# Kernel tuning notes

Hardware: AMD Instinct MI355X
Metric: run time of the kernel (lower is better)

## Reference

```python
import jax, jax.numpy as jnp
import numpy as np

B, S, BERT_H = 8, 512, 432
NL, HD = 12, 64
H = NL * HD  # 768
NEG = -1e12

def _lin(k, i, o):
    return jax.random.normal(k, (i, o), jnp.float32) * 0.02

def setup_inputs():
    key = jax.random.key(0)
    ks = jax.random.split(key, 12)
    return {
        "bert_hidden": jax.random.normal(ks[0], (B, S, BERT_H), jnp.float32),
        "attention_mask": jnp.ones((B, S), jnp.float32),
        "dense_w": _lin(ks[1], BERT_H, H), "dense_b": jnp.zeros((H,)),
        "sat_qw": _lin(ks[2], H, H), "sat_qb": jnp.zeros((H,)),
        "sat_kw": _lin(ks[3], H, H), "sat_kb": jnp.zeros((H,)),
        "sat_vw": _lin(ks[4], H, H), "sat_vb": jnp.zeros((H,)),
        "sat_ow": _lin(ks[5], H, H), "sat_ob": jnp.zeros((H,)),
        "rel_qw": _lin(ks[6], H, H), "rel_qb": jnp.zeros((H,)),
        "rel_kw": _lin(ks[7], H, H), "rel_kb": jnp.zeros((H,)),
        "rel_vw": _lin(ks[8], H, H), "rel_vb": jnp.zeros((H,)),
        "rel_ow": _lin(ks[9], H, H), "rel_ob": jnp.zeros((H,)),
        "lns_w": jnp.ones((H,)), "lns_b": jnp.zeros((H,)),
        "lnr_w": jnp.ones((H,)), "lnr_b": jnp.zeros((H,)),
        "head_w": _lin(ks[10], H, 2 * HD), "head_b": jnp.zeros((2 * HD,)),
        "tail_w": _lin(ks[11], 2 * HD, 2 * NL), "tail_b": jnp.zeros((2 * NL,)),
    }

def _layernorm(x, w, b, eps=1e-12):
    u = x.mean(-1, keepdims=True)
    s = ((x - u) ** 2).mean(-1, keepdims=True)
    return w * (x - u) / jnp.sqrt(s + eps) + b

def _mha(q_in, k_in, v_in, wq, bq, wk, bk, wv, bv, wo, bo):
    # q_in: [N, Lq, H]; k_in/v_in: [N, Lk, H]; dropout is identity (eval)
    N, Lq, _ = q_in.shape
    Lk = k_in.shape[1]
    qh = (q_in @ wq + bq).reshape(N, Lq, NL, HD)
    kh = (k_in @ wk + bk).reshape(N, Lk, NL, HD)
    vh = (v_in @ wv + bv).reshape(N, Lk, NL, HD)
    scores = jnp.einsum('nqhd,nkhd->nhqk', qh, kh) / np.float32(np.sqrt(HD))
    probs = jax.nn.softmax(scores, axis=-1)
    ctx = jnp.einsum('nhqk,nkhd->nqhd', probs, vh).reshape(N, Lq, NL * HD)
    return ctx @ wo + bo + q_in

def _shift_back(x):
    # faithful torch cycle_shift(forward=False): circular roll left by 1
    return jnp.roll(x, -1, axis=1)

def _shift_fwd(x):
    # faithful to the torch sequential in-place loop in cycle_shift(forward=True):
    # out[0] = x[-1]; out[1:] = x[0] (each copy reads the already-overwritten slot)
    b, s, h = x.shape
    return jnp.concatenate([x[:, -1:, :], jnp.broadcast_to(x[:, :1, :], (b, s - 1, h))], axis=1)

def reference(bert_hidden, attention_mask, dense_w, dense_b,
              sat_qw, sat_qb, sat_kw, sat_kb, sat_vw, sat_vb, sat_ow, sat_ob,
              rel_qw, rel_qb, rel_kw, rel_kb, rel_vw, rel_vb, rel_ow, rel_ob,
              lns_w, lns_b, lnr_w, lnr_b, head_w, head_b, tail_w, tail_b):
    hidden0 = bert_hidden @ dense_w + dense_b  # [B,S,H]
    cs = hidden0
    center = cs.mean(axis=1)  # [B,H], avg_pool2d over seq dim
    for _ in range(2):
        before = _shift_back(cs)
        after = _shift_fwd(cs)
        center_exp = jnp.broadcast_to(center[:, None, :], cs.shape)
        concats = jnp.stack([before, cs, after, hidden0, center_exp], axis=2)  # [B,S,5,H]
        concats = concats.reshape(B * S, 5, H)
        q = cs.reshape(B * S, 1, H)
        sat = _mha(q, concats, concats, sat_qw, sat_qb, sat_kw, sat_kb, sat_vw, sat_vb, sat_ow, sat_ob)
        cs = _layernorm(jax.nn.relu(sat), lns_w, lns_b).reshape(B, S, H)
        cc = jnp.concatenate([center[:, None, :], cs], axis=1)  # [B,S+1,H]
        rel = _mha(center[:, None, :], cc, cc, rel_qw, rel_qb, rel_kw, rel_kb, rel_vw, rel_vb, rel_ow, rel_ob)
        center = _layernorm(jax.nn.relu(rel), lnr_w, lnr_b)[:, 0, :]
    outputs = cs @ head_w + head_b  # [B,S,2*HD]
    qw, kw = outputs[..., ::2], outputs[..., 1::2]  # [B,S,HD]
    pos = jnp.arange(S, dtype=jnp.float32)
    inv = jnp.power(10000.0, -2.0 * jnp.arange(HD // 2, dtype=jnp.float32) / HD)
    ang = pos[:, None] * inv[None, :]  # [S,HD//2]
    pe = jnp.stack([jnp.sin(ang), jnp.cos(ang)], axis=-1).reshape(S, HD)
    cos_pos = jnp.repeat(pe[:, 1::2], 2, axis=-1)  # [S,HD]
    sin_pos = jnp.repeat(pe[:, ::2], 2, axis=-1)
    def rot(x):
        x2 = jnp.stack([-x[..., 1::2], x[..., ::2]], axis=-1).reshape(x.shape)
        return x * cos_pos + x2 * sin_pos
    qw, kw = rot(qw), rot(kw)
    logits = jnp.einsum('bmd,bnd->bmn', qw, kw) / np.float32(np.sqrt(HD))  # [B,S,S]
    bias = jnp.einsum('bnh->bhn', outputs @ tail_w + tail_b) / 2.0  # [B,2*NL,S]
    logits = logits[:, None, :, :] + bias[:, ::2, None, :] + bias[:, 1::2, :, None]  # [B,NL,S,S]
    m1 = attention_mask[:, None, :, None]
    logits = logits * m1 + NEG * (1.0 - m1)
    m2 = attention_mask[:, None, None, :]
    logits = logits * m2 + NEG * (1.0 - m2)
    tril = jnp.tril(jnp.ones((S, S), logits.dtype), k=-1)
    return logits - tril * 1e12
```

## Files before the change

kernel.cpp:

```cpp
#include <hip/hip_runtime.h>
#include <cstdint>
#include <cstddef>

#define HH 768
#define SS 512
#define NBATCH 8
#define NLH 12
#define HDIM 64
#define BSROWS 4096
static constexpr float NEGV = -1000000000000.0f;

typedef unsigned short ushort_t;
typedef __attribute__((ext_vector_type(4))) float fx4;
typedef __attribute__((ext_vector_type(8))) short sx8;

__device__ __forceinline__ ushort_t f2bf(float f) {
  uint32_t u = __float_as_uint(f);
  uint32_t r = (u + 0x7FFFu + ((u >> 16) & 1u)) >> 16;
  return (ushort_t)r;
}
__device__ __forceinline__ float bf2f(ushort_t h) {
  return __uint_as_float(((uint32_t)h) << 16);
}
__device__ __forceinline__ float2 ldbf2(const ushort_t* p) {
  uint32_t u = *(const uint32_t*)p;
  return make_float2(__uint_as_float(u << 16), __uint_as_float(u & 0xffff0000u));
}

__device__ __forceinline__ void async_copy16(void* lds, const void* g) {
  __builtin_amdgcn_global_load_lds(
      (const __attribute__((address_space(1))) void*)g,
      (__attribute__((address_space(3))) void*)lds, 16, 0, 0);
}

__device__ __forceinline__ void gemm_core(
    char* arena, int bid, int nwg, int nx,
    const ushort_t* __restrict__ A, int lda,
    const ushort_t* __restrict__ B, int ldb,
    const float* __restrict__ bias,
    const ushort_t* __restrict__ resb,
    ushort_t* __restrict__ Cb, int ldo,
    ushort_t* __restrict__ Cb2, int ldo2, int nsplit, int K,
    float* __restrict__ colmean)
{
  ushort_t* As = (ushort_t*)arena;
  ushort_t* Bs = (ushort_t*)(arena + 16384);
  const int tid = threadIdx.x;
  const int q = nwg >> 3;
  const int xcd = bid & 7, sidx = bid >> 3;
  const int swz = xcd * q + sidx;
  const int bm = (swz / nx) * 128;
  const int bn = (swz % nx) * 128;
  const int l = tid & 63;
  const int w = tid >> 6;
  const int wr = w >> 1, wc = w & 1;
  const int r8 = tid >> 3;
  const int sl = tid & 7;

  fx4 acc[4][4];
#pragma unroll
  for (int m = 0; m < 4; ++m)
#pragma unroll
    for (int n = 0; n < 4; ++n) acc[m][n] = (fx4)0.f;

  for (int k0 = 0; k0 < K; k0 += 64) {
#pragma unroll
    for (int i = 0; i < 4; ++i) {
      int row = i * 32 + r8;
      int srcs = sl ^ (row & 7);
      async_copy16((char*)As + i * 4096 + tid * 16,
                   A + (size_t)(bm + row) * lda + k0 + srcs * 8);
    }
#pragma unroll
    for (int i = 0; i < 4; ++i) {
      int row = i * 32 + r8;
      int srcs = sl ^ (row & 7);
      async_copy16((char*)Bs + i * 4096 + tid * 16,
                   B + (size_t)(bn + row) * ldb + k0 + srcs * 8);
    }
    __syncthreads();
#pragma unroll
    for (int kk = 0; kk < 2; ++kk) {
      sx8 av[4], bv[4];
      const int so = (l >> 4) + kk * 4;
#pragma unroll
      for (int m = 0; m < 4; ++m) {
        int r = wr * 64 + m * 16 + (l & 15);
        av[m] = *(const sx8*)((const char*)As + r * 128 + ((so ^ (r & 7)) * 16));
      }
#pragma unroll
      for (int n = 0; n < 4; ++n) {
        int r = wc * 64 + n * 16 + (l & 15);
        bv[n] = *(const sx8*)((const char*)Bs + r * 128 + ((so ^ (r & 7)) * 16));
      }
#pragma unroll
      for (int m = 0; m < 4; ++m)
#pragma unroll
        for (int n = 0; n < 4; ++n)
          acc[m][n] = __builtin_amdgcn_mfma_f32_16x16x32_bf16(av[m], bv[n], acc[m][n], 0, 0, 0);
    }
    __syncthreads();
  }

  const bool second = (bn >= nsplit);
  ushort_t* dst = second ? Cb2 : Cb;
  const int ld = second ? ldo2 : ldo;
  const int csub = second ? nsplit : 0;
  const int cr0 = bm + wr * 64 + (l >> 4) * 4;
  const int cc0 = bn + wc * 64 + (l & 15);
#pragma unroll
  for (int m = 0; m < 4; ++m) {
#pragma unroll
    for (int n = 0; n < 4; ++n) {
      int col = cc0 + n * 16;
      float bcol = bias[col];
#pragma unroll
      for (int j = 0; j < 4; ++j) {
        int row = cr0 + m * 16 + j;
        size_t off = (size_t)row * ld + (col - csub);
        float v = acc[m][n][j] + bcol;
        if (resb) v += bf2f(resb[off]);
        dst[off] = f2bf(v);
      }
    }
  }

  if (colmean) {
    float* scr = (float*)arena;
    const int cid = wr * 4 + (l >> 4);
#pragma unroll
    for (int n = 0; n < 4; ++n) {
      int colL = wc * 64 + n * 16 + (l & 15);
      float t = 16.0f * bias[bn + colL];
#pragma unroll
      for (int m = 0; m < 4; ++m)
#pragma unroll
        for (int j = 0; j < 4; ++j) t += acc[m][n][j];
      scr[cid * 128 + colL] = t;
    }
    __syncthreads();
    if (tid < 128) {
      float scol = 0.f;
#pragma unroll
      for (int c = 0; c < 8; ++c) scol += scr[c * 128 + tid];
      atomicAdd(&colmean[(bm >> 9) * HH + bn + tid], scol * (1.0f / 512.0f));
    }
  }
}

struct SmallJob { const float* W; const float* bias; const float* res; float* C; };
struct SmallJobs { SmallJob j[5]; };

__device__ __forceinline__ void skinny_core(
    char* arena, int colblk,
    const float* __restrict__ A, const float* __restrict__ W,
    const float* __restrict__ bias, const float* __restrict__ res, float* __restrict__ C)
{
  float* As = (float*)arena;
  float* part = (float*)(arena + 24576);
  const int tid = threadIdx.x;
#pragma unroll
  for (int i = 0; i < 6; ++i) {
    int idx = tid * 4 + i * 1024;
    *(float4*)&As[idx] = *(const float4*)(A + idx);
  }
  __syncthreads();
  const int c = tid & 31;
  const int col = (colblk << 5) + c;
  const int ks = tid >> 5;
  const float* Wp = W + (size_t)(ks * 96) * HH + col;
  float acc[8] = {};
#pragma unroll 8
  for (int k = 0; k < 96; ++k) {
    float wv = Wp[(size_t)k * HH];
    const float* ap = &As[ks * 96 + k];
#pragma unroll
    for (int m = 0; m < 8; ++m)
      acc[m] = fmaf(ap[m * HH], wv, acc[m]);
  }
#pragma unroll
  for (int m = 0; m < 8; ++m)
    part[ks * 256 + m * 32 + c] = acc[m];
  __syncthreads();
  const int m = tid >> 5;
  const int c2 = tid & 31;
  float s = 0.f;
#pragma unroll
  for (int k = 0; k < 8; ++k) s += part[k * 256 + m * 32 + c2];
  const int outcol = (colblk << 5) + c2;
  float v = s + bias[outcol];
  if (res) v += res[(size_t)m * HH + outcol];
  C[(size_t)m * HH + outcol] = v;
}

__global__ __launch_bounds__(256) void gemm_bf16(
    const ushort_t* __restrict__ A, int lda,
    const ushort_t* __restrict__ B, int ldb,
    const float* __restrict__ bias,
    const ushort_t* __restrict__ resb,
    ushort_t* __restrict__ Cb, int ldo,
    ushort_t* __restrict__ Cb2, int ldo2, int nsplit, int K, int nx,
    float* __restrict__ colmean)
{
  __shared__ char arena[32768];
  gemm_core(arena, blockIdx.x, gridDim.x, nx, A, lda, B, ldb, bias, resb,
            Cb, ldo, Cb2, ldo2, nsplit, K, colmean);
}

__global__ __launch_bounds__(256) void qkv_center(
    const ushort_t* __restrict__ A, const ushort_t* __restrict__ B,
    const float* __restrict__ bias, ushort_t* __restrict__ Cb,
    SmallJobs jobs, const float* __restrict__ center)
{
  __shared__ char arena[32768];
  if (blockIdx.x < 576) {
    gemm_core(arena, blockIdx.x, 576, 18, A, HH, B, HH, bias, nullptr,
              Cb, 2304, nullptr, 0, 1 << 30, HH, nullptr);
  } else {
    int vb = blockIdx.x - 576;
    SmallJob jb = jobs.j[vb / 24];
    skinny_core(arena, vb % 24, center, jb.W, jb.bias, jb.res, jb.C);
  }
}

__global__ __launch_bounds__(256) void gemm_skinny(
    const float* __restrict__ A, SmallJobs jobs)
{
  __shared__ char arena[32768];
  SmallJob jb = jobs.j[blockIdx.y];
  skinny_core(arena, blockIdx.x, A, jb.W, jb.bias, jb.res, jb.C);
}

struct SmallJobs2 { SmallJob j[2]; };
__global__ __launch_bounds__(256) void skinny_ln(
    const float* __restrict__ relo, const float* __restrict__ lw, const float* __restrict__ lb,
    SmallJobs2 jobs)
{
  __shared__ float As[8 * HH];
  __shared__ float part[8 * 8 * 32];
  const int tid = threadIdx.x;
  const SmallJob job = jobs.j[blockIdx.y];
#pragma unroll
  for (int i = 0; i < 6; ++i) {
    int idx = tid * 4 + i * 1024;
    *(float4*)&As[idx] = *(const float4*)(relo + idx);
  }
  __syncthreads();
  {
    const int row = tid >> 5, lc = tid & 31;
    float s = 0.f, sq = 0.f;
#pragma unroll
    for (int e = 0; e < 24; ++e) {
      float x = fmaxf(As[row * HH + lc * 24 + e], 0.f);
      s += x; sq += x * x;
    }
#pragma unroll
    for (int d = 1; d < 32; d <<= 1) { s += __shfl_xor(s, d); sq += __shfl_xor(sq, d); }
    float mean = s * (1.0f / HH);
    float var = sq * (1.0f / HH) - mean * mean;
    float rstd = rsqrtf(var + 1e-12f);
#pragma unroll
    for (int e = 0; e < 24; ++e) {
      int cc = lc * 24 + e;
      float x = fmaxf(As[row * HH + cc], 0.f);
      As[row * HH + cc] = lw[cc] * (x - mean) * rstd + lb[cc];
    }
  }
  __syncthreads();
  const int c = tid & 31;
  const int col = (blockIdx.x << 5) + c;
  const int ks = tid >> 5;
  const float* Wp = job.W + (size_t)(ks * 96) * HH + col;
  float acc[8] = {};
#pragma unroll 8
  for (int k = 0; k < 96; ++k) {
    float wv = Wp[(size_t)k * HH];
    const float* ap = &As[ks * 96 + k];
#pragma unroll
    for (int m = 0; m < 8; ++m)
      acc[m] = fmaf(ap[m * HH], wv, acc[m]);
  }
#pragma unroll
  for (int m = 0; m < 8; ++m)
    part[ks * 256 + m * 32 + c] = acc[m];
  __syncthreads();
  const int m = tid >> 5;
  const int c2 = tid & 31;
  float s2 = 0.f;
#pragma unroll
  for (int k = 0; k < 8; ++k) s2 += part[k * 256 + m * 32 + c2];
  const int outcol = (blockIdx.x << 5) + c2;
  job.C[(size_t)m * HH + outcol] = s2 + job.bias[outcol];
}

__global__ __launch_bounds__(256) void rel_attn(
    const float* __restrict__ Qr, const float* __restrict__ Krc, const ushort_t* __restrict__ Kr,
    const float* __restrict__ Vrc, const ushort_t* __restrict__ Vr, int ldkv,
    float* __restrict__ ctx)
{
  int b = blockIdx.x, h = blockIdx.y;
  __shared__ float qs[64];
  __shared__ float sc[513];
  __shared__ float part[4][64];
  __shared__ float redm[4], redsum[4];
  int t = threadIdx.x, lane = t & 63, wave = t >> 6;
  if (t < 64) qs[t] = Qr[b * HH + h * HDIM + t];
  __syncthreads();
  for (int j = t; j < 513; j += 256) {
    float acc = 0.f;
    if (j == 0) {
      const float* kp = Krc + b * HH + h * HDIM;
#pragma unroll
      for (int d = 0; d < HDIM; ++d) acc = fmaf(qs[d], kp[d], acc);
    } else {
      const sx8* kv = (const sx8*)(Kr + (size_t)(b * SS + j - 1) * ldkv + h * HDIM);
#pragma unroll
      for (int dq = 0; dq < 8; ++dq) {
        sx8 v = kv[dq];
#pragma unroll
        for (int e = 0; e < 8; ++e)
          acc = fmaf(qs[dq * 8 + e], bf2f((ushort_t)v[e]), acc);
      }
    }
    sc[j] = acc * 0.125f;
  }
  __syncthreads();
  float m = -1e30f;
  for (int j = t; j < 513; j += 256) m = fmaxf(m, sc[j]);
#pragma unroll
  for (int d = 1; d < 64; d <<= 1) m = fmaxf(m, __shfl_xor(m, d));
  if (lane == 0) redm[wave] = m;
  __syncthreads();
  m = fmaxf(fmaxf(redm[0], redm[1]), fmaxf(redm[2], redm[3]));
  float lsum = 0.f;
  for (int j = t; j < 513; j += 256) { float e = __expf(sc[j] - m); sc[j] = e; lsum += e; }
#pragma unroll
  for (int d = 1; d < 64; d <<= 1) lsum += __shfl_xor(lsum, d);
  if (lane == 0) redsum[wave] = lsum;
  __syncthreads();
  float total = redsum[0] + redsum[1] + redsum[2] + redsum[3];
  float accv = 0.f;
#pragma unroll 8
  for (int j = wave; j < 513; j += 4) {
    float vv = (j == 0) ? Vrc[b * HH + h * HDIM + lane]
                        : bf2f(Vr[(size_t)(b * SS + j - 1) * ldkv + h * HDIM + lane]);
    accv = fmaf(sc[j], vv, accv);
  }
  part[wave][lane] = accv;
  __syncthreads();
  if (wave == 0) {
    float r = (part[0][lane] + part[1][lane] + part[2][lane] + part[3][lane]) / total;
    ctx[b * HH + h * HDIM + lane] = r;
  }
}

__global__ __launch_bounds__(256) void head_fused(
    const ushort_t* __restrict__ Araw,
    const float* __restrict__ lnw, const float* __restrict__ lnb,
    const ushort_t* __restrict__ B,
    const float* __restrict__ head_b,
    const float* __restrict__ tail_w,
    const float* __restrict__ tail_b,
    float* __restrict__ qw, float* __restrict__ kw,
    float* __restrict__ bias2)
{
  __shared__ ushort_t As[128 * 64];
  __shared__ ushort_t Bs[128 * 64];
  __shared__ float tile[128][130];
  __shared__ float invt[32];
  __shared__ float2 rst[128];
  const int tid = threadIdx.x;
  const int bm = blockIdx.x * 128;
  const int l = tid & 63;
  const int w = tid >> 6;
  const int wr = w >> 1, wc = w & 1;
  const int r8 = tid >> 3;
  const int sl = tid & 7;

  if (tid < 32) invt[tid] = powf(10000.0f, -(float)tid / 32.0f);

  {
    int row = tid >> 1, half = tid & 1;
    const ushort_t* rp = Araw + (size_t)(bm + row) * HH + half * 384;
    float s = 0.f, sq = 0.f;
#pragma unroll 8
    for (int c = 0; c < 48; ++c) {
      sx8 v = *(const sx8*)(rp + c * 8);
#pragma unroll
      for (int e = 0; e < 8; ++e) {
        float x = fmaxf(bf2f((ushort_t)v[e]), 0.f);
        s += x; sq += x * x;
      }
    }
    s += __shfl_xor(s, 1); sq += __shfl_xor(sq, 1);
    if (half == 0) {
      float mean = s * (1.0f / HH);
      float var = sq * (1.0f / HH) - mean * mean;
      rst[row] = make_float2(mean, rsqrtf(var + 1e-12f));
    }
  }
  __syncthreads();

  fx4 acc[4][4];
#pragma unroll
  for (int m = 0; m < 4; ++m)
#pragma unroll
    for (int n = 0; n < 4; ++n) acc[m][n] = (fx4)0.f;

  for (int k0 = 0; k0 < HH; k0 += 64) {
#pragma unroll
    for (int i = 0; i < 4; ++i) {
      int row = i * 32 + r8;
      int srcs = sl ^ (row & 7);
      async_copy16((char*)Bs + i * 4096 + tid * 16,
                   B + (size_t)row * HH + k0 + srcs * 8);
    }
#pragma unroll
    for (int i = 0; i < 4; ++i) {
      int row = i * 32 + r8;
      int slot = sl ^ (row & 7);
      int gk = k0 + slot * 8;
      sx8 v = *(const sx8*)(Araw + (size_t)(bm + row) * HH + gk);
      float4 w0 = *(const float4*)(lnw + gk);
      float4 w1 = *(const float4*)(lnw + gk + 4);
      float4 b0 = *(const float4*)(lnb + gk);
      float4 b1 = *(const float4*)(lnb + gk + 4);
      float wv[8] = {w0.x, w0.y, w0.z, w0.w, w1.x, w1.y, w1.z, w1.w};
      float bv[8] = {b0.x, b0.y, b0.z, b0.w, b1.x, b1.y, b1.z, b1.w};
      float2 mr = rst[row];
      sx8 ov;
#pragma unroll
      for (int e = 0; e < 8; ++e) {
        float x = fmaxf(bf2f((ushort_t)v[e]), 0.f);
        ov[e] = (short)f2bf(fmaf((x - mr.x) * mr.y, wv[e], bv[e]));
      }
      *(sx8*)((char*)As + i * 4096 + tid * 16) = ov;
    }
    __syncthreads();
#pragma unroll
    for (int kk = 0; kk < 2; ++kk) {
      sx8 av[4], bvv[4];
      const int so = (l >> 4) + kk * 4;
#pragma unroll
      for (int m = 0; m < 4; ++m) {
        int r = wr * 64 + m * 16 + (l & 15);
        av[m] = *(const sx8*)((const char*)As + r * 128 + ((so ^ (r & 7)) * 16));
      }
#pragma unroll
      for (int n = 0; n < 4; ++n) {
        int r = wc * 64 + n * 16 + (l & 15);
        bvv[n] = *(const sx8*)((const char*)Bs + r * 128 + ((so ^ (r & 7)) * 16));
      }
#pragma unroll
      for (int m = 0; m < 4; ++m)
#pragma unroll
        for (int n = 0; n < 4; ++n)
          acc[m][n] = __builtin_amdgcn_mfma_f32_16x16x32_bf16(av[m], bvv[n], acc[m][n], 0, 0, 0);
    }
    __syncthreads();
  }

  const int cr0 = wr * 64 + (l >> 4) * 4;
  const int cc0 = wc * 64 + (l & 15);
#pragma unroll
  for (int m = 0; m < 4; ++m)
#pragma unroll
    for (int n = 0; n < 4; ++n) {
      int col = cc0 + n * 16;
      float bcol = head_b[col];
#pragma unroll
      for (int j = 0; j < 4; ++j)
        tile[cr0 + m * 16 + j][col] = acc[m][n][j] + bcol;
    }
  __syncthreads();

  for (int t = tid; t < 128 * 32; t += 256) {
    int r = t >> 5, i = t & 31;
    int s = (bm + r) & 511;
    float ang = (float)s * invt[i];
    float sn = sinf(ang), cn = cosf(ang);
    float q0 = tile[r][4 * i + 0], k0 = tile[r][4 * i + 1];
    float q1 = tile[r][4 * i + 2], k1 = tile[r][4 * i + 3];
    float* qp = qw + (size_t)(bm + r) * 64 + i * 2;
    float* kp = kw + (size_t)(bm + r) * 64 + i * 2;
    qp[0] = q0 * cn - q1 * sn; qp[1] = q1 * cn + q0 * sn;
    kp[0] = k0 * cn - k1 * sn; kp[1] = k1 * cn + k0 * sn;
  }
  for (int t = tid; t < 128 * 24; t += 256) {
    int r = t / 24, c = t % 24;
    float acc2 = tail_b[c];
#pragma unroll 16
    for (int k = 0; k < 128; ++k) acc2 = fmaf(tile[r][k], tail_w[k * 24 + c], acc2);
    bias2[(size_t)(bm + r) * 24 + c] = acc2 * 0.5f;
  }
}

struct TJob { const float* src; ushort_t* dst; int K, N, Kpad, rowOff; };
struct PrepArgs {
  TJob j[8];
  const float* bert; ushort_t* bert_bf;
  const float* rkb; const float* rvb; const float* sqb; const float* skb; const float* svb;
  float* b_merged;
  float* center;
};
__global__ __launch_bounds__(256) void prep_all(PrepArgs pa)
{
  if (blockIdx.z < 8) {
    TJob jb = pa.j[blockIdx.z];
    int k0 = blockIdx.x * 32, n0 = blockIdx.y * 32;
    if (k0 >= jb.Kpad || n0 >= jb.N) return;
    __shared__ float t[32][33];
    int tx = threadIdx.x & 31, ty = threadIdx.x >> 5;
#pragma unroll
    for (int i = 0; i < 4; ++i) {
      int k = k0 + ty + i * 8;
      float v = 0.f;
      if (k < jb.K && n0 + tx < jb.N) v = jb.src[(size_t)k * jb.N + n0 + tx];
      t[ty + i * 8][tx] = v;
    }
    __syncthreads();
#pragma unroll
    for (int i = 0; i < 4; ++i) {
      int n = n0 + ty + i * 8;
      int k = k0 + tx;
      if (n < jb.N && k < jb.Kpad)
        jb.dst[(size_t)(jb.rowOff + n) * jb.Kpad + k] = f2bf(t[tx][ty + i * 8]);
    }
  } else {
    const int NB = BSROWS * 448;
    const int total = NB + 3840 + NBATCH * HH;
    int start = (blockIdx.y * 24 + blockIdx.x) * 256 + threadIdx.x;
    for (int i = start; i < total; i += 24 * 24 * 256) {
      if (i < NB) {
        int r = i / 448, c = i % 448;
        pa.bert_bf[i] = (c < 432) ? f2bf(pa.bert[(size_t)r * 432 + c]) : (ushort_t)0;
      } else if (i < NB + 3840) {
        int c = i - NB;
        float v;
        if (c < 768) v = pa.rkb[c];
        else if (c < 1536) v = pa.rvb[c - 768];
        else if (c < 2304) v = pa.sqb[c - 1536];
        else if (c < 3072) v = pa.skb[c - 2304];
        else v = pa.svb[c - 3072];
        pa.b_merged[c] = v;
      } else {
        pa.center[i - NB - 3840] = 0.f;
      }
    }
  }
}

__global__ __launch_bounds__(256) void sat_attn(
    const ushort_t* __restrict__ Qc, const ushort_t* __restrict__ Kc,
    const ushort_t* __restrict__ Vc, int ldq,
    const ushort_t* __restrict__ Kh0, const ushort_t* __restrict__ Vh0, int ldh,
    const float* __restrict__ Kcen, const float* __restrict__ Vcen,
    ushort_t* __restrict__ ctxb)
{
  int i = blockIdx.x;
  int b = i >> 9, s = i & 511;
  int lane = threadIdx.x & 63;
  int wave = threadIdx.x >> 6;
  size_t rb = (size_t)(b * SS + ((s + 1) & 511));
  size_t rs = (size_t)i;
  size_t ra = (size_t)(b * SS + (s == 0 ? (SS - 1) : 0));
  size_t rc = (size_t)b * HH;
  const int half = lane >> 5;
  const int d0 = (lane & 31) * 2;
#pragma unroll
  for (int it = 0; it < 2; ++it) {
    int p = wave + 4 * it;
    if (p >= 6) break;
    int off = (2 * p + half) * HDIM + d0;
    float2 q  = ldbf2(Qc + rs * ldq + off);
    float2 kb = ldbf2(Kc + rb * ldq + off);
    float2 ks = ldbf2(Kc + rs * ldq + off);
    float2 ka = ldbf2(Kc + ra * ldq + off);
    float2 kh = ldbf2(Kh0 + rs * ldh + off);
    float2 kc = *(const float2*)(Kcen + rc + off);
    float s0 = q.x * kb.x + q.y * kb.y;
    float s1 = q.x * ks.x + q.y * ks.y;
    float s2 = q.x * ka.x + q.y * ka.y;
    float s3 = q.x * kh.x + q.y * kh.y;
    float s4 = q.x * kc.x + q.y * kc.y;
#pragma unroll
    for (int d = 1; d < 32; d <<= 1) {
      s0 += __shfl_xor(s0, d); s1 += __shfl_xor(s1, d); s2 += __shfl_xor(s2, d);
      s3 += __shfl_xor(s3, d); s4 += __shfl_xor(s4, d);
    }
    const float sc = 0.125f;
    s0 *= sc; s1 *= sc; s2 *= sc; s3 *= sc; s4 *= sc;
    float mx = fmaxf(fmaxf(fmaxf(s0, s1), fmaxf(s2, s3)), s4);
    float e0 = __expf(s0 - mx), e1 = __expf(s1 - mx), e2 = __expf(s2 - mx);
    float e3 = __expf(s3 - mx), e4 = __expf(s4 - mx);
    float inv = 1.f / (e0 + e1 + e2 + e3 + e4);
    float2 vb = ldbf2(Vc + rb * ldq + off);
    float2 vs = ldbf2(Vc + rs * ldq + off);
    float2 va = ldbf2(Vc + ra * ldq + off);
    float2 vh = ldbf2(Vh0 + rs * ldh + off);
    float2 vc = *(const float2*)(Vcen + rc + off);
    float vx = e0 * vb.x + e1 * vs.x + e2 * va.x + e3 * vh.x + e4 * vc.x;
    float vy = e0 * vb.y + e1 * vs.y + e2 * va.y + e3 * vh.y + e4 * vc.y;
    uint32_t o = (uint32_t)f2bf(vx * inv) | ((uint32_t)f2bf(vy * inv) << 16);
    *(uint32_t*)(ctxb + rs * HH + off) = o;
  }
}

__global__ __launch_bounds__(256) void relu_ln_bf(
    const ushort_t* __restrict__ x, const float* __restrict__ w, const float* __restrict__ b,
    ushort_t* __restrict__ ybf)
{
  int row = blockIdx.x;
  const ushort_t* xr = x + (size_t)row * HH;
  float v[3];
  float sum = 0.f, sumsq = 0.f;
#pragma unroll
  for (int j = 0; j < 3; ++j) {
    float t = bf2f(xr[threadIdx.x + j * 256]);
    t = fmaxf(t, 0.f);
    v[j] = t;
    sum += t; sumsq += t * t;
  }
#pragma unroll
  for (int d = 1; d < 64; d <<= 1) { sum += __shfl_xor(sum, d); sumsq += __shfl_xor(sumsq, d); }
  __shared__ float ws_[4], wsq_[4];
  int wave = threadIdx.x >> 6, lane = threadIdx.x & 63;
  if (lane == 0) { ws_[wave] = sum; wsq_[wave] = sumsq; }
  __syncthreads();
  sum = ws_[0] + ws_[1] + ws_[2] + ws_[3];
  sumsq = wsq_[0] + wsq_[1] + wsq_[2] + wsq_[3];
  float mean = sum * (1.0f / HH);
  float var = sumsq * (1.0f / HH) - mean * mean;
  float rstd = rsqrtf(var + 1e-12f);
#pragma unroll
  for (int j = 0; j < 3; ++j) {
    int cidx = threadIdx.x + j * 256;
    float o = w[cidx] * (v[j] - mean) * rstd + b[cidx];
    ybf[(size_t)row * HH + cidx] = f2bf(o);
  }
}

__global__ __launch_bounds__(256) void final_kernel(
    const float* __restrict__ qw, const float* __restrict__ kw,
    const float* __restrict__ bias2, const float* __restrict__ mask,
    float* __restrict__ out)
{
  int b = blockIdx.z;
  int mt = blockIdx.y * 32;
  int nt = blockIdx.x * 32;
  __shared__ float qs[32][68];
  __shared__ float ks[32][68];
  int t = threadIdx.x;
  {
    int idx = t * 8;
    int r = idx >> 6, c = idx & 63;
    const float* sq = qw + (size_t)(b * SS + mt + r) * 64 + c;
    const float* sk = kw + (size_t)(b * SS + nt + r) * 64 + c;
    *(float4*)&qs[r][c]     = *(const float4*)(sq);
    *(float4*)&qs[r][c + 4] = *(const float4*)(sq + 4);
    *(float4*)&ks[r][c]     = *(const float4*)(sk);
    *(float4*)&ks[r][c + 4] = *(const float4*)(sk + 4);
  }
  __syncthreads();
  int m = t >> 3;
  int n0 = (t & 7) * 4;
  float d0 = 0.f, d1 = 0.f, d2 = 0.f, d3 = 0.f;
#pragma unroll
  for (int d = 0; d < 64; d += 4) {
    float4 qv = *(const float4*)&qs[m][d];
    float4 k0 = *(const float4*)&ks[n0 + 0][d];
    float4 k1 = *(const float4*)&ks[n0 + 1][d];
    float4 k2 = *(const float4*)&ks[n0 + 2][d];
    float4 k3 = *(const float4*)&ks[n0 + 3][d];
    d0 += qv.x * k0.x + qv.y * k0.y + qv.z * k0.z + qv.w * k0.w;
    d1 += qv.x * k1.x + qv.y * k1.y + qv.z * k1.z + qv.w * k1.w;
    d2 += qv.x * k2.x + qv.y * k2.y + qv.z * k2.z + qv.w * k2.w;
    d3 += qv.x * k3.x + qv.y * k3.y + qv.z * k3.z + qv.w * k3.w;
  }
  int gm = mt + m;
  int gn = nt + n0;
  d0 *= 0.125f; d1 *= 0.125f; d2 *= 0.125f; d3 *= 0.125f;
  float mm = mask[b * SS + gm];
  float mn0 = mask[b * SS + gn + 0];
  float mn1 = mask[b * SS + gn + 1];
  float mn2 = mask[b * SS + gn + 2];
  float mn3 = mask[b * SS + gn + 3];
  const float* bmp  = bias2 + (size_t)(b * SS + gm) * 24;
  const float* bnp0 = bias2 + (size_t)(b * SS + gn + 0) * 24;
  const float* bnp1 = bias2 + (size_t)(b * SS + gn + 1) * 24;
  const float* bnp2 = bias2 + (size_t)(b * SS + gn + 2) * 24;
  const float* bnp3 = bias2 + (size_t)(b * SS + gn + 3) * 24;
#pragma unroll
  for (int h = 0; h < NLH; ++h) {
    float tb = bmp[2 * h + 1];
    float v0 = d0 + bnp0[2 * h] + tb;
    float v1 = d1 + bnp1[2 * h] + tb;
    float v2 = d2 + bnp2[2 * h] + tb;
    float v3 = d3 + bnp3[2 * h] + tb;
    v0 = v0 * mm + NEGV * (1.f - mm); v1 = v1 * mm + NEGV * (1.f - mm);
    v2 = v2 * mm + NEGV * (1.f - mm); v3 = v3 * mm + NEGV * (1.f - mm);
    v0 = v0 * mn0 + NEGV * (1.f - mn0); v1 = v1 * mn1 + NEGV * (1.f - mn1);
    v2 = v2 * mn2 + NEGV * (1.f - mn2); v3 = v3 * mn3 + NEGV * (1.f - mn3);
    if (gm > gn + 0) v0 -= 1000000000000.0f;
    if (gm > gn + 1) v1 -= 1000000000000.0f;
    if (gm > gn + 2) v2 -= 1000000000000.0f;
    if (gm > gn + 3) v3 -= 1000000000000.0f;
    float4 o = make_float4(v0, v1, v2, v3);
    *(float4*)(out + ((((size_t)(b * NLH + h)) * SS + gm) * SS + gn)) = o;
  }
}

extern "C" void kernel_launch(void* const* d_in, const int* in_sizes, int n_in,
                              void* d_out, int out_size, void* d_ws, size_t ws_size,
                              hipStream_t stream)
{
  const float* bert    = (const float*)d_in[0];
  const float* amask   = (const float*)d_in[1];
  const float* dense_w = (const float*)d_in[2];
  const float* dense_b = (const float*)d_in[3];
  const float* sat_qw  = (const float*)d_in[4];
  const float* sat_qb  = (const float*)d_in[5];
  const float* sat_kw  = (const float*)d_in[6];
  const float* sat_kb  = (const float*)d_in[7];
  const float* sat_vw  = (const float*)d_in[8];
  const float* sat_vb  = (const float*)d_in[9];
  const float* sat_ow  = (const float*)d_in[10];
  const float* sat_ob  = (const float*)d_in[11];
  const float* rel_qw  = (const float*)d_in[12];
  const float* rel_qb  = (const float*)d_in[13];
  const float* rel_kw  = (const float*)d_in[14];
  const float* rel_kb  = (const float*)d_in[15];
  const float* rel_vw  = (const float*)d_in[16];
  const float* rel_vb  = (const float*)d_in[17];
  const float* rel_ow  = (const float*)d_in[18];
  const float* rel_ob  = (const float*)d_in[19];
  const float* lns_w   = (const float*)d_in[20];
  const float* lns_b   = (const float*)d_in[21];
  const float* lnr_w   = (const float*)d_in[22];
  const float* lnr_b   = (const float*)d_in[23];
  const float* head_w  = (const float*)d_in[24];
  const float* head_b  = (const float*)d_in[25];
  const float* tail_w  = (const float*)d_in[26];
  const float* tail_b  = (const float*)d_in[27];

  float* out = (float*)d_out;
  char*  ws  = (char*)d_ws;

  size_t off = 0;
  auto alloc = [&](size_t bytes) { char* p = ws + off; off += (bytes + 255) & ~(size_t)255; return p; };
  ushort_t* bert_bf   = (ushort_t*)alloc((size_t)BSROWS * 448 * 2);
  ushort_t* Wt_dense  = (ushort_t*)alloc((size_t)768 * 448 * 2);
  ushort_t* Wt_big    = (ushort_t*)alloc((size_t)3840 * 768 * 2);
  ushort_t* Wt_satow  = (ushort_t*)alloc((size_t)768 * 768 * 2);
  ushort_t* Wt_head   = (ushort_t*)alloc((size_t)128 * 768 * 2);
  ushort_t* hidden0_bf= (ushort_t*)alloc((size_t)BSROWS * HH * 2);
  ushort_t* ctx_bf    = (ushort_t*)alloc((size_t)BSROWS * HH * 2);
  ushort_t* csA_bf    = (ushort_t*)alloc((size_t)BSROWS * HH * 2);
  float* b_merged = (float*)alloc(3840 * 4);
  float* center   = (float*)alloc(6144 * 4);
  float* Kcen     = (float*)alloc(6144 * 4);
  float* Vcen     = (float*)alloc(6144 * 4);
  float* Qr       = (float*)alloc(6144 * 4);
  float* Krc      = (float*)alloc(6144 * 4);
  float* Vrc      = (float*)alloc(6144 * 4);
  float* ctxr     = (float*)alloc(6144 * 4);
  float* relo     = (float*)alloc(6144 * 4);
  float* bias2    = (float*)alloc((size_t)BSROWS * 24 * 4);
  float* qwbuf    = (float*)alloc((size_t)BSROWS * 64 * 4);
  float* kwbuf    = (float*)alloc((size_t)BSROWS * 64 * 4);

  ushort_t* QKV1_bf = (ushort_t*)out;
  ushort_t* tmp1_bf = QKV1_bf + (size_t)BSROWS * 2304;
  ushort_t* KrVr_bf = tmp1_bf + (size_t)BSROWS * 768;
  ushort_t* QKV2_bf = KrVr_bf + (size_t)BSROWS * 1536;
  ushort_t* tmp2_bf = tmp1_bf;

  dim3 blk(256);

  {
    PrepArgs pa;
    pa.j[0] = { dense_w, Wt_dense, 432, 768, 448, 0 };
    pa.j[1] = { rel_kw,  Wt_big,   768, 768, 768, 0 };
    pa.j[2] = { rel_vw,  Wt_big,   768, 768, 768, 768 };
    pa.j[3] = { sat_qw,  Wt_big,   768, 768, 768, 1536 };
    pa.j[4] = { sat_kw,  Wt_big,   768, 768, 768, 2304 };
    pa.j[5] = { sat_vw,  Wt_big,   768, 768, 768, 3072 };
    pa.j[6] = { sat_ow,  Wt_satow, 768, 768, 768, 0 };
    pa.j[7] = { head_w,  Wt_head,  768, 128, 768, 0 };
    pa.bert = bert; pa.bert_bf = bert_bf;
    pa.rkb = rel_kb; pa.rvb = rel_vb; pa.sqb = sat_qb; pa.skb = sat_kb; pa.svb = sat_vb;
    pa.b_merged = b_merged; pa.center = center;
    prep_all<<<dim3(24, 24, 9), blk, 0, stream>>>(pa);
  }

  gemm_bf16<<<dim3(192), blk, 0, stream>>>(bert_bf, 448, Wt_dense, 448, dense_b,
                                           nullptr, hidden0_bf, HH,
                                           nullptr, 0, 1 << 30, 448, 6, center);

  {
    SmallJobs jobs;
    jobs.j[0] = { sat_kw, sat_kb, nullptr, Kcen };
    jobs.j[1] = { sat_vw, sat_vb, nullptr, Vcen };
    jobs.j[2] = { rel_qw, rel_qb, nullptr, Qr };
    jobs.j[3] = { rel_kw, rel_kb, nullptr, Krc };
    jobs.j[4] = { rel_vw, rel_vb, nullptr, Vrc };
    qkv_center<<<dim3(696), blk, 0, stream>>>(hidden0_bf, Wt_big + (size_t)1536 * 768,
                                              b_merged + 1536, QKV1_bf, jobs, center);
  }
  sat_attn<<<BSROWS, 256, 0, stream>>>(QKV1_bf, QKV1_bf + 768, QKV1_bf + 1536, 2304,
                                       QKV1_bf + 768, QKV1_bf + 1536, 2304,
                                       Kcen, Vcen, ctx_bf);
  gemm_bf16<<<dim3(192), blk, 0, stream>>>(ctx_bf, HH, Wt_satow, HH, sat_ob,
                                           hidden0_bf, tmp1_bf, HH,
                                           nullptr, 0, 1 << 30, HH, 6, nullptr);
  relu_ln_bf<<<BSROWS, 256, 0, stream>>>(tmp1_bf, lns_w, lns_b, csA_bf);

  gemm_bf16<<<dim3(960), blk, 0, stream>>>(csA_bf, HH, Wt_big, HH, b_merged,
                                           nullptr, KrVr_bf, 1536,
                                           QKV2_bf, 2304, 1536, HH, 30, nullptr);
  rel_attn<<<dim3(8, 12), 256, 0, stream>>>(Qr, Krc, KrVr_bf, Vrc, KrVr_bf + 768, 1536, ctxr);
  {
    SmallJobs jobs;
    jobs.j[0] = { rel_ow, rel_ob, center, relo };
    gemm_skinny<<<dim3(24, 1), blk, 0, stream>>>(ctxr, jobs);
  }
  {
    SmallJobs2 jobs;
    jobs.j[0] = { sat_kw, sat_kb, nullptr, Kcen };
    jobs.j[1] = { sat_vw, sat_vb, nullptr, Vcen };
    skinny_ln<<<dim3(24, 2), blk, 0, stream>>>(relo, lnr_w, lnr_b, jobs);
  }
  sat_attn<<<BSROWS, 256, 0, stream>>>(QKV2_bf, QKV2_bf + 768, QKV2_bf + 1536, 2304,
                                       QKV1_bf + 768, QKV1_bf + 1536, 2304,
                                       Kcen, Vcen, ctx_bf);
  gemm_bf16<<<dim3(192), blk, 0, stream>>>(ctx_bf, HH, Wt_satow, HH, sat_ob,
                                           csA_bf, tmp2_bf, HH,
                                           nullptr, 0, 1 << 30, HH, 6, nullptr);
  head_fused<<<32, blk, 0, stream>>>(tmp2_bf, lns_w, lns_b, Wt_head, head_b,
                                     tail_w, tail_b, qwbuf, kwbuf, bias2);
  final_kernel<<<dim3(16, 16, 8), 256, 0, stream>>>(qwbuf, kwbuf, bias2, amask, out);
}
```

Before: 306.7 us.

## Shrink head_fused row tile to 16 rows and launch 256 blocks

```diff
diff --git a/kernel.cpp b/kernel.cpp
--- a/kernel.cpp
+++ b/kernel.cpp
@@ -364,27 +364,26 @@
     float* __restrict__ qw, float* __restrict__ kw,
     float* __restrict__ bias2)
 {
-  __shared__ ushort_t As[128 * 64];
+  __shared__ ushort_t As[16 * 64];
   __shared__ ushort_t Bs[128 * 64];
-  __shared__ float tile[128][130];
+  __shared__ float tile[16][130];
   __shared__ float invt[32];
-  __shared__ float2 rst[128];
+  __shared__ float2 rst[16];
   const int tid = threadIdx.x;
-  const int bm = blockIdx.x * 128;
+  const int bm = blockIdx.x * 16;
   const int l = tid & 63;
   const int w = tid >> 6;
-  const int wr = w >> 1, wc = w & 1;
   const int r8 = tid >> 3;
   const int sl = tid & 7;
 
   if (tid < 32) invt[tid] = powf(10000.0f, -(float)tid / 32.0f);
 
   {
-    int row = tid >> 1, half = tid & 1;
-    const ushort_t* rp = Araw + (size_t)(bm + row) * HH + half * 384;
+    int row = tid >> 4, part = tid & 15;
+    const ushort_t* rp = Araw + (size_t)(bm + row) * HH + part * 48;
     float s = 0.f, sq = 0.f;
-#pragma unroll 8
-    for (int c = 0; c < 48; ++c) {
+#pragma unroll
+    for (int c = 0; c < 6; ++c) {
       sx8 v = *(const sx8*)(rp + c * 8);
 #pragma unroll
       for (int e = 0; e < 8; ++e) {
@@ -392,8 +391,9 @@
         s += x; sq += x * x;
       }
     }
-    s += __shfl_xor(s, 1); sq += __shfl_xor(sq, 1);
-    if (half == 0) {
+#pragma unroll
+    for (int d = 1; d < 16; d <<= 1) { s += __shfl_xor(s, d); sq += __shfl_xor(sq, d); }
+    if (part == 0) {
       float mean = s * (1.0f / HH);
       float var = sq * (1.0f / HH) - mean * mean;
       rst[row] = make_float2(mean, rsqrtf(var + 1e-12f));
@@ -401,11 +401,8 @@
   }
   __syncthreads();
 
-  fx4 acc[4][4];
-#pragma unroll
-  for (int m = 0; m < 4; ++m)
-#pragma unroll
-    for (int n = 0; n < 4; ++n) acc[m][n] = (fx4)0.f;
+  fx4 acc[2];
+  acc[0] = (fx4)0.f; acc[1] = (fx4)0.f;
 
   for (int k0 = 0; k0 < HH; k0 += 64) {
 #pragma unroll
@@ -415,9 +412,8 @@
       async_copy16((char*)Bs + i * 4096 + tid * 16,
                    B + (size_t)row * HH + k0 + srcs * 8);
     }
-#pragma unroll
-    for (int i = 0; i < 4; ++i) {
-      int row = i * 32 + r8;
+    if (tid < 128) {
+      int row = tid >> 3;
       int slot = sl ^ (row & 7);
       int gk = k0 + slot * 8;
       sx8 v = *(const sx8*)(Araw + (size_t)(bm + row) * HH + gk);
@@ -434,47 +430,40 @@
         float x = fmaxf(bf2f((ushort_t)v[e]), 0.f);
         ov[e] = (short)f2bf(fmaf((x - mr.x) * mr.y, wv[e], bv[e]));
       }
-      *(sx8*)((char*)As + i * 4096 + tid * 16) = ov;
+      *(sx8*)((char*)As + row * 128 + sl * 16) = ov;
     }
     __syncthreads();
 #pragma unroll
     for (int kk = 0; kk < 2; ++kk) {
-      sx8 av[4], bvv[4];
       const int so = (l >> 4) + kk * 4;
-#pragma unroll
-      for (int m = 0; m < 4; ++m) {
-        int r = wr * 64 + m * 16 + (l & 15);
-        av[m] = *(const sx8*)((const char*)As + r * 128 + ((so ^ (r & 7)) * 16));
+      int ra = l & 15;
+      sx8 av = *(const sx8*)((const char*)As + ra * 128 + ((so ^ (ra & 7)) * 16));
+#pragma unroll
+      for (int n = 0; n < 2; ++n) {
+        int r = w * 32 + n * 16 + (l & 15);
+        sx8 bv = *(const sx8*)((const char*)Bs + r * 128 + ((so ^ (r & 7)) * 16));
+        acc[n] = __builtin_amdgcn_mfma_f32_16x16x32_bf16(av, bv, acc[n], 0, 0, 0);
       }
-#pragma unroll
-      for (int n = 0; n < 4; ++n) {
-        int r = wc * 64 + n * 16 + (l & 15);
-        bvv[n] = *(const sx8*)((const char*)Bs + r * 128 + ((so ^ (r & 7)) * 16));
-      }
-#pragma unroll
-      for (int m = 0; m < 4; ++m)
-#pragma unroll
-        for (int n = 0; n < 4; ++n)
-          acc[m][n] = __builtin_amdgcn_mfma_f32_16x16x32_bf16(av[m], bvv[n], acc[m][n], 0, 0, 0);
     }
     __syncthreads();
   }
 
-  const int cr0 = wr * 64 + (l >> 4) * 4;
-  const int cc0 = wc * 64 + (l & 15);
-#pragma unroll
-  for (int m = 0; m < 4; ++m)
-#pragma unroll
-    for (int n = 0; n < 4; ++n) {
-      int col = cc0 + n * 16;
+  {
+    const int rr0 = (l >> 4) * 4;
+#pragma unroll
+    for (int n = 0; n < 2; ++n) {
+      int col = w * 32 + n * 16 + (l & 15);
       float bcol = head_b[col];
 #pragma unroll
       for (int j = 0; j < 4; ++j)
-        tile[cr0 + m * 16 + j][col] = acc[m][n][j] + bcol;
-    }
-  __syncthreads();
-
-  for (int t = tid; t < 128 * 32; t += 256) {
+        tile[rr0 + j][col] = acc[n][j] + bcol;
+    }
+  }
+  __syncthreads();
+
+#pragma unroll
+  for (int it = 0; it < 2; ++it) {
+    int t = tid + it * 256;
     int r = t >> 5, i = t & 31;
     int s = (bm + r) & 511;
     float ang = (float)s * invt[i];
@@ -486,7 +475,7 @@
     qp[0] = q0 * cn - q1 * sn; qp[1] = q1 * cn + q0 * sn;
     kp[0] = k0 * cn - k1 * sn; kp[1] = k1 * cn + k0 * sn;
   }
-  for (int t = tid; t < 128 * 24; t += 256) {
+  for (int t = tid; t < 16 * 24; t += 256) {
     int r = t / 24, c = t % 24;
     float acc2 = tail_b[c];
 #pragma unroll 16
@@ -836,7 +825,7 @@
   gemm_bf16<<<dim3(192), blk, 0, stream>>>(ctx_bf, HH, Wt_satow, HH, sat_ob,
                                            csA_bf, tmp2_bf, HH,
                                            nullptr, 0, 1 << 30, HH, 6, nullptr);
-  head_fused<<<32, blk, 0, stream>>>(tmp2_bf, lns_w, lns_b, Wt_head, head_b,
-                                     tail_w, tail_b, qwbuf, kwbuf, bias2);
+  head_fused<<<256, blk, 0, stream>>>(tmp2_bf, lns_w, lns_b, Wt_head, head_b,
+                                      tail_w, tail_b, qwbuf, kwbuf, bias2);
   final_kernel<<<dim3(16, 16, 8), 256, 0, stream>>>(qwbuf, kwbuf, bias2, amask, out);
 }
```

After: 266.0 us. 1.15x faster.
